# Optimization experiments

Hardware: AMD Instinct MI355X
Metric: run time of the kernel (lower is better)

Reference implementation:

```python
import jax, jax.numpy as jnp
import numpy as np

DIM = 512
NUM_HEADS = 8
HEAD_DIM = DIM // NUM_HEADS


def setup_inputs() -> dict:
    key = jax.random.key(0)
    k_x, k_qkv, k_p = jax.random.split(key, 3)
    b, n, c = 8, 4096, DIM
    x = jax.random.normal(k_x, (b, n, c), dtype=jnp.float32)
    # xavier_uniform for Linear(dim, 3*dim): limit = sqrt(6/(in+out))
    lim_qkv = float(np.sqrt(6.0 / (c + 3 * c)))
    w_qkv = jax.random.uniform(k_qkv, (c, 3 * c), dtype=jnp.float32, minval=-lim_qkv, maxval=lim_qkv)
    b_qkv = jnp.zeros((3 * c,), dtype=jnp.float32)
    lim_p = float(np.sqrt(6.0 / (c + c)))
    w_p = jax.random.uniform(k_p, (c, c), dtype=jnp.float32, minval=-lim_p, maxval=lim_p)
    b_p = jnp.zeros((c,), dtype=jnp.float32)
    temperature = jnp.full((NUM_HEADS, 1, 1), 1.0 / np.sqrt(HEAD_DIM), dtype=jnp.float32)
    return {"x": x, "w_qkv": w_qkv, "b_qkv": b_qkv, "w_p": w_p, "b_p": b_p,
            "temperature": temperature}


def reference(x, w_qkv, b_qkv, w_p, b_p, temperature):
    b, n, c = x.shape
    h, d = NUM_HEADS, HEAD_DIM
    qkv = x @ w_qkv + b_qkv                      # [b, n, 3c]
    q, k, v = jnp.split(qkv, 3, axis=-1)         # each [b, n, c]
    # -> [b, h, n, d]
    q = q.reshape(b, n, h, d).transpose(0, 2, 1, 3)
    k = k.reshape(b, n, h, d).transpose(0, 2, 1, 3)
    v = v.reshape(b, n, h, d).transpose(0, 2, 1, 3)
    # channel attention: d x d score matrix, reduced over tokens n
    scores = jnp.einsum('bhnd,bhne->bhde', q, k) * temperature  # [b,h,d,d]
    attn = jax.nn.softmax(scores, axis=-1)
    # y = attn @ v^T then permute -> [b, n, h, d]
    y = jnp.einsum('bhde,bhne->bnhd', attn, v).reshape(b, n, c)
    return y @ w_p + b_p
```

## Files before the change

### kernel.cpp

```cpp
#include <hip/hip_runtime.h>

typedef __attribute__((ext_vector_type(8))) short s16x8;
typedef __attribute__((ext_vector_type(4))) short s16x4;
typedef __attribute__((ext_vector_type(4))) float fx4;

__device__ inline unsigned short f2bf(float f) {
  unsigned u = __float_as_uint(f);
  u += 0x7fffu + ((u >> 16) & 1u);
  return (unsigned short)(u >> 16);
}
__device__ inline float bf2f(unsigned short s) {
  return __uint_as_float(((unsigned)s) << 16);
}

#define GLDS16(gp, lp) \
  __builtin_amdgcn_global_load_lds((const __attribute__((address_space(1))) void*)(gp), \
                                   (__attribute__((address_space(3))) void*)(lp), 16, 0, 0)

__global__ __launch_bounds__(256) void cast_x_k(const float* __restrict__ x,
                                                unsigned short* __restrict__ xb,
                                                unsigned short* __restrict__ xT,
                                                float* __restrict__ s_part,
                                                const float* __restrict__ w,
                                                const float* __restrict__ wp,
                                                unsigned short* __restrict__ wkT,
                                                unsigned short* __restrict__ wvb,
                                                unsigned short* __restrict__ wpb) {
  __shared__ unsigned short lt[64 * 66];
  __shared__ float red[64 * 4];
  int blk = blockIdx.x;
  int t = threadIdx.x;
  if (blk >= 4096) {
    int wblk = blk - 4096;
    if (wblk < 64) {
      int rt = wblk >> 3, ct = wblk & 7;
      int rn = t >> 2, seg = (t & 3) * 16;
      const float* src = w + (size_t)(ct * 64 + rn) * 1536 + 512 + rt * 64 + seg;
#pragma unroll
      for (int k = 0; k < 16; ++k) lt[(seg + k) * 66 + rn] = f2bf(src[k]);
      __syncthreads();
      int j = t >> 2, nseg = (t & 3) * 16;
      unsigned short* o = wkT + (size_t)(rt * 64 + j) * 512 + ct * 64 + nseg;
      *(s16x8*)&o[0] = *(s16x8*)&lt[j * 66 + nseg];
      *(s16x8*)&o[8] = *(s16x8*)&lt[j * 66 + nseg + 8];
    } else if (wblk < 192) {
      int o = (wblk - 64) * 2048 + t * 8;
      int c = o >> 9, e = o & 511;
      const float* src = w + (size_t)c * 1536 + 1024 + e;
      unsigned short h[8];
#pragma unroll
      for (int i = 0; i < 8; ++i) h[i] = f2bf(src[i]);
      *(s16x8*)&wvb[o] = *(s16x8*)&h[0];
    } else {
      int o = (wblk - 192) * 2048 + t * 8;
      unsigned short h[8];
#pragma unroll
      for (int i = 0; i < 8; ++i) h[i] = f2bf(wp[o + i]);
      *(s16x8*)&wpb[o] = *(s16x8*)&h[0];
    }
    return;
  }
  int b = blk >> 9, r = blk & 511, nt = r >> 3, ct = r & 7;
  int n0 = nt * 64, c0 = ct * 64;
  int rn = t >> 2, seg = (t & 3) * 16;
  const float* xp = x + ((size_t)b * 4096 + n0 + rn) * 512 + c0 + seg;
  fx4 v0 = *(const fx4*)&xp[0], v1 = *(const fx4*)&xp[4];
  fx4 v2 = *(const fx4*)&xp[8], v3 = *(const fx4*)&xp[12];
  unsigned short h[16];
  h[0]=f2bf(v0[0]); h[1]=f2bf(v0[1]); h[2]=f2bf(v0[2]); h[3]=f2bf(v0[3]);
  h[4]=f2bf(v1[0]); h[5]=f2bf(v1[1]); h[6]=f2bf(v1[2]); h[7]=f2bf(v1[3]);
  h[8]=f2bf(v2[0]); h[9]=f2bf(v2[1]); h[10]=f2bf(v2[2]); h[11]=f2bf(v2[3]);
  h[12]=f2bf(v3[0]); h[13]=f2bf(v3[1]); h[14]=f2bf(v3[2]); h[15]=f2bf(v3[3]);
  unsigned short* xbo = xb + ((size_t)b * 4096 + n0 + rn) * 512 + c0 + seg;
  *(s16x8*)&xbo[0] = *(s16x8*)&h[0];
  *(s16x8*)&xbo[8] = *(s16x8*)&h[8];
#pragma unroll
  for (int k = 0; k < 16; ++k) lt[(seg + k) * 66 + rn] = h[k];
  __syncthreads();
  {
    int c = t & 63, q = t >> 6;
    float p = 0.f;
#pragma unroll
    for (int i = 0; i < 16; ++i) p += bf2f(lt[c * 66 + q * 16 + i]);
    red[c * 4 + q] = p;
  }
  __syncthreads();
  if (t < 64) {
    float s = red[t * 4] + red[t * 4 + 1] + red[t * 4 + 2] + red[t * 4 + 3];
    s_part[((size_t)(b * 64 + nt)) * 512 + c0 + t] = s;
  }
  int c = t >> 2, nseg = (t & 3) * 16;
  unsigned short* xto = xT + ((size_t)b * 512 + c0 + c) * 4096 + n0 + nseg;
  *(s16x8*)&xto[0] = *(s16x8*)&lt[c * 66 + nseg];
  *(s16x8*)&xto[8] = *(s16x8*)&lt[c * 66 + nseg + 8];
}

template <int MODE>
__global__ __launch_bounds__(256, 4) void gemm_k(
    const unsigned short* __restrict__ A0, const unsigned short* __restrict__ B0,
    const float* __restrict__ bias, unsigned short* __restrict__ obf,
    float* __restrict__ of32, const float* __restrict__ wf) {
  constexpr int LD = (MODE == 0) ? 4096 : 512;
  constexpr int KSTEPS = (MODE == 0) ? 32 : 16;
  constexpr int NWG = (MODE == 0) ? 352 : (MODE == 3) ? 1024 : (MODE == 2) ? 136 : 128;
  __shared__ alignas(16) unsigned short As[2][128 * 32];
  __shared__ alignas(16) unsigned short Bs[2][128 * 32];
  int tid = threadIdx.x, wave = tid >> 6, lane = tid & 63;
  int l15 = lane & 15, l16 = lane >> 4;
  int wr = wave >> 1, wc = wave & 1;

  int bid = (blockIdx.x & 7) * (NWG >> 3) + (blockIdx.x >> 3);

  if (MODE == 0 && bid >= 320) {
    float* sb = (float*)As;
    int ubid = bid - 320;
    int b = ubid >> 2, jq = ubid & 3;
    int t = tid;
#pragma unroll
    for (int cc = 0; cc < 2; ++cc) {
      int c = cc * 256 + t;
      float a = 0.f;
      for (int nt = 0; nt < 64; ++nt)
        a += bias[((size_t)(b * 64 + nt)) * 512 + c];
      sb[c] = a;
    }
    __syncthreads();
    int j = jq * 256 + t;
    float ua = 0.f;
    for (int c = 0; c < 512; ++c)
      ua += sb[c] * wf[(size_t)c * 1536 + j];
    ((float*)obf)[b * 1024 + j] = ua;
    return;
  }
  if (MODE == 2 && bid >= 128) {
    float* bv = (float*)As;
    int b = bid - 128;
    int t = tid;
    bv[t] = bias[1024 + t];
    bv[t + 256] = bias[1280 + t];
    __syncthreads();
#pragma unroll
    for (int jj = 0; jj < 2; ++jj) {
      int j = jj * 256 + t;
      const unsigned short* wrow = &A0[((size_t)(b * 512 + j)) << 9];
      float s = 0.f;
      for (int e = 0; e < 512; e += 8) {
        s16x8 v = *(const s16x8*)&wrow[e];
#pragma unroll
        for (int q = 0; q < 8; ++q) s += bv[e + q] * bf2f((unsigned short)v[q]);
      }
      of32[b * 512 + j] = wf[j] + s;
    }
    return;
  }

  int b = 0, mt = 0, nt = 0, ks = 0;
  if (MODE == 0) {
    const int TTM[10] = {0, 0, 0, 0, 1, 1, 1, 2, 2, 3};
    const int TTN[10] = {0, 1, 2, 3, 1, 2, 3, 2, 3, 3};
    ks = bid / 80; int r = bid - ks * 80; b = r / 10; int tt = r - b * 10;
    mt = TTM[tt]; nt = TTN[tt];
  }
  else if (MODE == 3) { b = bid >> 7; int r = bid & 127; mt = r >> 2; nt = r & 3; }
  else { b = bid >> 4; mt = (bid >> 2) & 3; nt = bid & 3; }

  const unsigned short* Ab;
  const unsigned short* Bb;
  if (MODE == 0) { Ab = A0 + ((size_t)b * 512 + mt * 128) * 4096 + ks * 1024;
                   Bb = A0 + ((size_t)b * 512 + nt * 128) * 4096 + ks * 1024; }
  else if (MODE == 1) { Ab = A0 + (size_t)mt * 128 * 512;
                        Bb = B0 + ((size_t)b * 512 + nt * 128) * 512; }
  else if (MODE == 2) { Ab = A0 + ((size_t)b * 512 + mt * 128) * 512;
                        Bb = B0 + (size_t)nt * 128 * 512; }
  else { Ab = A0 + ((size_t)b * 4096 + mt * 128) * 512;
         Bb = B0 + ((size_t)b * 512 + nt * 128) * 512; }

  fx4 acc[4][4];
#pragma unroll
  for (int i = 0; i < 4; ++i)
#pragma unroll
    for (int j = 0; j < 4; ++j) acc[i][j] = (fx4){0.f, 0.f, 0.f, 0.f};

  int smr = wave * 16 + (lane >> 2);
  int skk = (((lane & 3) ^ ((lane >> 3) & 3))) * 8;
  const unsigned short* agp = Ab + (size_t)smr * LD + skk;
  const unsigned short* bgp = Bb + (size_t)smr * LD + skk;
  int ldsoff = wave * 512;

#define STAGE(buf, kt_)                                          \
  do {                                                           \
    int k0_ = (kt_) * 32;                                        \
    GLDS16(agp + k0_, &As[buf][ldsoff]);                         \
    GLDS16(agp + (size_t)64 * LD + k0_, &As[buf][ldsoff + 2048]);\
    GLDS16(bgp + k0_, &Bs[buf][ldsoff]);                         \
    GLDS16(bgp + (size_t)64 * LD + k0_, &Bs[buf][ldsoff + 2048]);\
  } while (0)

  STAGE(0, 0);
  asm volatile("s_waitcnt vmcnt(0)" ::: "memory");
  __builtin_amdgcn_s_barrier();

  int g = (l15 >> 1) & 3;
  int pa = (l16 ^ g) << 3;

  for (int kt = 0; kt < KSTEPS; ++kt) {
    int cur = kt & 1;
    if (kt < KSTEPS - 1) STAGE(cur ^ 1, kt + 1);

    s16x8 af[4], bf[4];
#pragma unroll
    for (int mi = 0; mi < 4; ++mi)
      af[mi] = *(const s16x8*)&As[cur][(wr * 64 + mi * 16 + l15) * 32 + pa];
#pragma unroll
    for (int nj = 0; nj < 4; ++nj)
      bf[nj] = *(const s16x8*)&Bs[cur][(wc * 64 + nj * 16 + l15) * 32 + pa];
#pragma unroll
    for (int mi = 0; mi < 4; ++mi)
#pragma unroll
      for (int nj = 0; nj < 4; ++nj)
        acc[mi][nj] = __builtin_amdgcn_mfma_f32_16x16x32_bf16(af[mi], bf[nj], acc[mi][nj], 0, 0, 0);

    asm volatile("s_waitcnt vmcnt(0)" ::: "memory");
    __builtin_amdgcn_s_barrier();
  }
#undef STAGE

  int R0 = mt * 128 + wr * 64, C0 = nt * 128 + wc * 64;
#pragma unroll
  for (int mi = 0; mi < 4; ++mi)
#pragma unroll
    for (int nj = 0; nj < 4; ++nj) {
      int gc = C0 + nj * 16 + l15;
#pragma unroll
      for (int r = 0; r < 4; ++r) {
        int gr = R0 + mi * 16 + l16 * 4 + r;
        float val = acc[mi][nj][r];
        if (MODE == 0) {
          of32[(((size_t)(ks * 8 + b)) * 512 + gr) * 512 + gc] = val;
        } else if (MODE == 1) {
          obf[((size_t)(b * 512 + gr)) * 512 + gc] = f2bf(val);
        } else if (MODE == 2) {
          obf[((size_t)(b * 512 + gr)) * 512 + gc] = f2bf(val);
        } else {
          of32[((size_t)(b * 4096 + gr)) * 512 + gc] = val + bias[b * 512 + gc];
        }
      }
    }
}

__global__ __launch_bounds__(256) void gsum_k(const float* __restrict__ Gpart,
                                              unsigned short* __restrict__ G16) {
  __shared__ float ts[64 * 65];
  int blk = blockIdx.x;
  int b = blk >> 6, rt = (blk >> 3) & 7, ct = blk & 7;
  int t = threadIdx.x;
  int r0 = t >> 4, c0 = (t & 15) * 4;
  bool lower = (rt >> 1) > (ct >> 1);
  if (!lower) {
#pragma unroll
    for (int rr = 0; rr < 4; ++rr) {
      int row = rr * 16 + r0;
      size_t base = (((size_t)b * 512) + rt * 64 + row) * 512 + ct * 64 + c0;
      fx4 a = {0.f, 0.f, 0.f, 0.f};
#pragma unroll
      for (int p = 0; p < 4; ++p) a += *(const fx4*)&Gpart[(size_t)p * 2097152 + base];
      unsigned short h4[4];
#pragma unroll
      for (int i = 0; i < 4; ++i) h4[i] = f2bf(a[i]);
      *(s16x4*)&G16[(((size_t)b * 512) + rt * 64 + row) * 512 + ct * 64 + c0] = *(s16x4*)&h4[0];
    }
  } else {
#pragma unroll
    for (int rr = 0; rr < 4; ++rr) {
      int srow = rr * 16 + r0;
      size_t base = (((size_t)b * 512) + ct * 64 + srow) * 512 + rt * 64 + c0;
      fx4 a = {0.f, 0.f, 0.f, 0.f};
#pragma unroll
      for (int p = 0; p < 4; ++p) a += *(const fx4*)&Gpart[(size_t)p * 2097152 + base];
#pragma unroll
      for (int i = 0; i < 4; ++i) ts[(c0 + i) * 65 + srow] = a[i];
    }
    __syncthreads();
#pragma unroll
    for (int rr = 0; rr < 4; ++rr) {
      int row = rr * 16 + r0;
      unsigned short h4[4];
#pragma unroll
      for (int i = 0; i < 4; ++i) h4[i] = f2bf(ts[row * 65 + c0 + i]);
      *(s16x4*)&G16[(((size_t)b * 512) + rt * 64 + row) * 512 + ct * 64 + c0] = *(s16x4*)&h4[0];
    }
  }
}

__global__ __launch_bounds__(256) void s_k(const float* __restrict__ wq,
                                           const unsigned short* __restrict__ GWT,
                                           float* __restrict__ sp) {
  __shared__ alignas(16) float Ws[64 * 68];
  __shared__ alignas(16) float Gs[64 * 68];
  int bid = blockIdx.x;
  int bh = bid >> 3, cch = bid & 7;
  int b = bh >> 3, h = bh & 7;
  int t = threadIdx.x;
  int cr = t >> 2, sg = (t & 3) * 16;
  const float* wsrc = wq + (size_t)(cch * 64 + cr) * 1536 + h * 64 + sg;
#pragma unroll
  for (int kk = 0; kk < 16; ++kk) Ws[cr * 68 + sg + kk] = wsrc[kk];
  const unsigned short* gsrc = GWT + ((size_t)b * 512 + h * 64 + cr) * 512 + cch * 64 + sg;
#pragma unroll
  for (int kk = 0; kk < 16; ++kk) Gs[(sg + kk) * 68 + cr] = bf2f(gsrc[kk]);
  __syncthreads();
  int dg = t >> 4, eg = t & 15;
  float acc[4][4] = {{0.f}};
  for (int cc = 0; cc < 64; ++cc) {
    fx4 wv = *(const fx4*)&Ws[cc * 68 + dg * 4];
    fx4 pv = *(const fx4*)&Gs[cc * 68 + eg * 4];
#pragma unroll
    for (int i = 0; i < 4; ++i)
#pragma unroll
      for (int j = 0; j < 4; ++j) acc[i][j] += wv[i] * pv[j];
  }
  float* o = sp + (size_t)bid * 4096;
#pragma unroll
  for (int i = 0; i < 4; ++i)
#pragma unroll
    for (int j = 0; j < 4; ++j) o[(dg * 4 + i) * 64 + eg * 4 + j] = acc[i][j];
}

__global__ __launch_bounds__(256) void softmax_weff_k(
    const float* __restrict__ sp, const unsigned short* __restrict__ wpb,
    const float* __restrict__ temp, const float* __restrict__ b_qkv,
    const float* __restrict__ u, unsigned short* __restrict__ weffT) {
  __shared__ alignas(16) float S[64 * 64];
  __shared__ alignas(16) unsigned short wps[64 * 128];
  int bh = blockIdx.x >> 2, jblk = blockIdx.x & 3;
  int b = bh >> 3, h = bh & 7;
  int tid = threadIdx.x;
  float tval = temp[h];
  for (int i = tid * 4; i < 4096; i += 1024) {
    fx4 s = {0.f, 0.f, 0.f, 0.f};
    for (int seg = 0; seg < 8; ++seg)
      s += *(const fx4*)&sp[((size_t)(bh * 8 + seg)) * 4096 + i];
    int d = i >> 6, e0 = i & 63;
    float bq = b_qkv[h * 64 + d];
    float uq = u[b * 1024 + h * 64 + d];
#pragma unroll
    for (int jj = 0; jj < 4; ++jj) {
      int e = e0 + jj;
      float bk = b_qkv[512 + h * 64 + e];
      float ksum = u[b * 1024 + 512 + h * 64 + e] + 4096.0f * bk;
      s[jj] += bq * ksum + bk * uq;
    }
    s *= tval;
    *(fx4*)&S[i] = s;
  }
  for (int i = tid * 8; i < 8192; i += 2048) {
    int d = i >> 7, c = i & 127;
    *(s16x8*)&wps[i] = *(const s16x8*)&wpb[(size_t)(h * 64 + d) * 512 + jblk * 128 + c];
  }
  __syncthreads();
  if (tid < 64) {
    float* row = &S[tid * 64];
    float mx = row[0];
    for (int e = 1; e < 64; ++e) mx = fmaxf(mx, row[e]);
    float sum = 0.f;
    for (int e = 0; e < 64; ++e) { float p = __expf(row[e] - mx); row[e] = p; sum += p; }
    float inv = 1.f / sum;
    for (int e = 0; e < 64; ++e) row[e] *= inv;
  }
  __syncthreads();
  int jg = tid >> 4, eg = tid & 15;
  int j0 = jg * 8;
  float a[4][8];
#pragma unroll
  for (int i = 0; i < 4; ++i)
#pragma unroll
    for (int j = 0; j < 8; ++j) a[i][j] = 0.f;
  for (int d = 0; d < 64; ++d) {
    fx4 at = *(const fx4*)&S[d * 64 + eg * 4];
    s16x8 wv = *(const s16x8*)&wps[d * 128 + j0];
    float wf8[8];
#pragma unroll
    for (int j = 0; j < 8; ++j) wf8[j] = bf2f((unsigned short)wv[j]);
#pragma unroll
    for (int i = 0; i < 4; ++i)
#pragma unroll
      for (int j = 0; j < 8; ++j) a[i][j] += at[i] * wf8[j];
  }
  int jglob = jblk * 128 + j0;
#pragma unroll
  for (int j = 0; j < 8; ++j) {
    unsigned short h4[4];
#pragma unroll
    for (int i = 0; i < 4; ++i) h4[i] = f2bf(a[i][j]);
    *(s16x4*)&weffT[(((size_t)b * 512 + jglob + j) << 9) + h * 64 + eg * 4] = *(s16x4*)&h4[0];
  }
}

extern "C" void kernel_launch(void* const* d_in, const int* in_sizes, int n_in,
                              void* d_out, int out_size, void* d_ws, size_t ws_size,
                              hipStream_t stream) {
  const float* x      = (const float*)d_in[0];
  const float* w_qkv  = (const float*)d_in[1];
  const float* b_qkv  = (const float*)d_in[2];
  const float* w_p    = (const float*)d_in[3];
  const float* b_p    = (const float*)d_in[4];
  const float* temp   = (const float*)d_in[5];
  float* out = (float*)d_out;
  char* ws = (char*)d_ws;

  unsigned short* xb     = (unsigned short*)(ws + 0);
  unsigned short* xT     = (unsigned short*)(ws + 33554432);
  float*          Gpart  = (float*)(ws + 67108864);
  float*          s_part = (float*)(ws + 67108864);
  unsigned short* G16    = (unsigned short*)(ws + 100663296);
  unsigned short* GWT    = (unsigned short*)(ws + 104857600);
  float*          sp     = (float*)(ws + 109051904);
  unsigned short* wkT    = (unsigned short*)(ws + 117440512);
  unsigned short* wvb    = (unsigned short*)(ws + 117964800);
  unsigned short* wpb    = (unsigned short*)(ws + 118489088);
  float*          u      = (float*)(ws + 119013376);
  float*          bias_o = (float*)(ws + 119046144);
  unsigned short* weffT  = (unsigned short*)(ws + 33554432);
  unsigned short* wcombT = (unsigned short*)(ws + 37748736);

  s_part = (float*)(ws + 119062528);

  cast_x_k<<<4416, 256, 0, stream>>>(x, xb, xT, s_part, w_qkv, w_p, wkT, wvb, wpb);
  gemm_k<0><<<352, 256, 0, stream>>>(xT, nullptr, s_part, (unsigned short*)u, Gpart, w_qkv);
  gsum_k<<<512, 256, 0, stream>>>(Gpart, G16);
  gemm_k<1><<<128, 256, 0, stream>>>(wkT, G16, nullptr, GWT, nullptr, nullptr);
  s_k<<<512, 256, 0, stream>>>(w_qkv, GWT, sp);
  softmax_weff_k<<<256, 256, 0, stream>>>(sp, wpb, temp, b_qkv, u, weffT);
  gemm_k<2><<<136, 256, 0, stream>>>(weffT, wvb, b_qkv, wcombT, bias_o, b_p);
  gemm_k<3><<<1024, 256, 0, stream>>>(xb, wcombT, bias_o, nullptr, out, nullptr);
}
```

Baseline: 137.2 us.

## Replace final output GEMM with 256x256-tile, 512-thread pipelined kernel

Moves the last GEMM (x times the combined weight, plus bias) out of the generic 128x128 gemm_k and into a dedicated kernel. The new kernel uses 256x256 tiles, 8 waves and BK=64 with an XOR-swizzled LDS layout. It splits global-to-LDS prefetches into quarter stages interleaved with MFMA groups under s_setprio, aiming for more reuse per loaded byte and better load/compute overlap. In exchange the grid drops to 256 workgroups with more LDS and registers per block, which lowers occupancy and adds many barriers.

```diff
diff --git a/kernel.cpp b/kernel.cpp
--- a/kernel.cpp
+++ b/kernel.cpp
@@ -102,7 +102,7 @@
     float* __restrict__ of32, const float* __restrict__ wf) {
   constexpr int LD = (MODE == 0) ? 4096 : 512;
   constexpr int KSTEPS = (MODE == 0) ? 32 : 16;
-  constexpr int NWG = (MODE == 0) ? 352 : (MODE == 3) ? 1024 : (MODE == 2) ? 136 : 128;
+  constexpr int NWG = (MODE == 0) ? 352 : (MODE == 2) ? 136 : 128;
   __shared__ alignas(16) unsigned short As[2][128 * 32];
   __shared__ alignas(16) unsigned short Bs[2][128 * 32];
   int tid = threadIdx.x, wave = tid >> 6, lane = tid & 63;
@@ -161,7 +161,6 @@
     ks = bid / 80; int r = bid - ks * 80; b = r / 10; int tt = r - b * 10;
     mt = TTM[tt]; nt = TTN[tt];
   }
-  else if (MODE == 3) { b = bid >> 7; int r = bid & 127; mt = r >> 2; nt = r & 3; }
   else { b = bid >> 4; mt = (bid >> 2) & 3; nt = bid & 3; }
 
   const unsigned short* Ab;
@@ -170,10 +169,8 @@
                    Bb = A0 + ((size_t)b * 512 + nt * 128) * 4096 + ks * 1024; }
   else if (MODE == 1) { Ab = A0 + (size_t)mt * 128 * 512;
                         Bb = B0 + ((size_t)b * 512 + nt * 128) * 512; }
-  else if (MODE == 2) { Ab = A0 + ((size_t)b * 512 + mt * 128) * 512;
-                        Bb = B0 + (size_t)nt * 128 * 512; }
-  else { Ab = A0 + ((size_t)b * 4096 + mt * 128) * 512;
-         Bb = B0 + ((size_t)b * 512 + nt * 128) * 512; }
+  else { Ab = A0 + ((size_t)b * 512 + mt * 128) * 512;
+         Bb = B0 + (size_t)nt * 128 * 512; }
 
   fx4 acc[4][4];
 #pragma unroll
@@ -237,13 +234,122 @@
         float val = acc[mi][nj][r];
         if (MODE == 0) {
           of32[(((size_t)(ks * 8 + b)) * 512 + gr) * 512 + gc] = val;
-        } else if (MODE == 1) {
+        } else {
           obf[((size_t)(b * 512 + gr)) * 512 + gc] = f2bf(val);
-        } else if (MODE == 2) {
-          obf[((size_t)(b * 512 + gr)) * 512 + gc] = f2bf(val);
-        } else {
-          of32[((size_t)(b * 4096 + gr)) * 512 + gc] = val + bias[b * 512 + gc];
         }
+      }
+    }
+}
+
+__global__ __launch_bounds__(512, 2) void gemm3_k(
+    const unsigned short* __restrict__ A0, const unsigned short* __restrict__ B0,
+    const float* __restrict__ bias, float* __restrict__ outp) {
+  __shared__ alignas(16) unsigned short As[2][16384];
+  __shared__ alignas(16) unsigned short Bs[2][16384];
+  int tid = threadIdx.x, wave = tid >> 6, lane = tid & 63;
+  int l15 = lane & 15, l16 = lane >> 4;
+  int wr = wave >> 2, wc = wave & 3;
+
+  int bid = (blockIdx.x & 7) * 32 + (blockIdx.x >> 3);
+  int b = bid >> 5, rr_ = bid & 31, mt = rr_ >> 1, nt = rr_ & 1;
+
+  const unsigned short* Ab = A0 + ((size_t)b * 4096 + mt * 256) * 512;
+  const unsigned short* Bb = B0 + ((size_t)b * 512 + nt * 256) * 512;
+
+  fx4 acc[8][4];
+#pragma unroll
+  for (int i = 0; i < 8; ++i)
+#pragma unroll
+    for (int j = 0; j < 4; ++j) acc[i][j] = (fx4){0.f, 0.f, 0.f, 0.f};
+
+  int srow = tid >> 3;
+  int chk = ((tid & 7) ^ (srow & 7)) * 8;
+  const unsigned short* agp = Ab + (size_t)srow * 512 + chk;
+  const unsigned short* bgp = Bb + (size_t)srow * 512 + chk;
+  int wofs = wave * 512;
+
+#define SG_A(nb, tt, h, q) GLDS16(agp + (size_t)((h)*128 + (q)*64) * 512 + (tt)*64, \
+                                  &As[nb][((h)*128 + (q)*64) * 64 + wofs])
+#define SG_B(nb, tt, h, q) GLDS16(bgp + (size_t)((h)*128 + (q)*64) * 512 + (tt)*64, \
+                                  &Bs[nb][((h)*128 + (q)*64) * 64 + wofs])
+
+  SG_A(0, 0, 0, 0); SG_A(0, 0, 0, 1); SG_A(0, 0, 1, 0); SG_A(0, 0, 1, 1);
+  SG_B(0, 0, 0, 0); SG_B(0, 0, 0, 1); SG_B(0, 0, 1, 0); SG_B(0, 0, 1, 1);
+
+  s16x8 af[4], bf[4];
+  int aro = wr * 128, bro = wc * 64;
+
+#define RD_A(buf, qm, ks)                                                              \
+  {                                                                                    \
+    _Pragma("unroll")                                                                  \
+    for (int i = 0; i < 4; ++i)                                                        \
+      af[i] = *(const s16x8*)&As[buf][(aro + (qm)*64 + i*16 + l15) * 64 +              \
+                                      ((((ks)*4 + l16) ^ (l15 & 7)) * 8)];             \
+  }
+#define RD_B(buf, ks)                                                                  \
+  {                                                                                    \
+    _Pragma("unroll")                                                                  \
+    for (int j = 0; j < 4; ++j)                                                        \
+      bf[j] = *(const s16x8*)&Bs[buf][(bro + j*16 + l15) * 64 +                        \
+                                      ((((ks)*4 + l16) ^ (l15 & 7)) * 8)];             \
+  }
+#define MM(qm)                                                                         \
+  {                                                                                    \
+    __builtin_amdgcn_s_setprio(1);                                                     \
+    _Pragma("unroll")                                                                  \
+    for (int i = 0; i < 4; ++i)                                                        \
+      _Pragma("unroll")                                                                \
+      for (int j = 0; j < 4; ++j)                                                      \
+        acc[(qm)*4 + i][j] =                                                           \
+            __builtin_amdgcn_mfma_f32_16x16x32_bf16(af[i], bf[j], acc[(qm)*4 + i][j], 0, 0, 0); \
+    __builtin_amdgcn_s_setprio(0);                                                     \
+  }
+
+  for (int t = 0; t < 8; ++t) {
+    int buf = t & 1, nb = buf ^ 1;
+    if (t < 7) {
+      SG_A(nb, t + 1, 0, 0); SG_A(nb, t + 1, 0, 1);
+      asm volatile("s_waitcnt vmcnt(2)" ::: "memory");
+    } else {
+      asm volatile("s_waitcnt vmcnt(0)" ::: "memory");
+    }
+    __builtin_amdgcn_s_barrier();
+    RD_A(buf, 0, 0); RD_B(buf, 0);
+    MM(0);
+    __builtin_amdgcn_s_barrier();
+    RD_A(buf, 1, 0);
+    if (t < 7) { SG_A(nb, t + 1, 1, 0); SG_A(nb, t + 1, 1, 1); }
+    __builtin_amdgcn_s_barrier();
+    MM(1);
+    __builtin_amdgcn_s_barrier();
+    RD_A(buf, 0, 1); RD_B(buf, 1);
+    if (t < 7) { SG_B(nb, t + 1, 0, 0); SG_B(nb, t + 1, 0, 1); }
+    __builtin_amdgcn_s_barrier();
+    MM(0);
+    __builtin_amdgcn_s_barrier();
+    RD_A(buf, 1, 1);
+    if (t < 7) { SG_B(nb, t + 1, 1, 0); SG_B(nb, t + 1, 1, 1); }
+    __builtin_amdgcn_s_barrier();
+    MM(1);
+    __builtin_amdgcn_s_barrier();
+  }
+#undef SG_A
+#undef SG_B
+#undef RD_A
+#undef RD_B
+#undef MM
+
+  int crow0 = mt * 256 + wr * 128, ccol0 = nt * 256 + wc * 64;
+#pragma unroll
+  for (int am = 0; am < 8; ++am)
+#pragma unroll
+    for (int nj = 0; nj < 4; ++nj) {
+      int gc = ccol0 + nj * 16 + l15;
+      float bsv = bias[b * 512 + gc];
+#pragma unroll
+      for (int r = 0; r < 4; ++r) {
+        int gr = crow0 + am * 16 + l16 * 4 + r;
+        outp[((size_t)(b * 4096 + gr)) * 512 + gc] = acc[am][nj][r] + bsv;
       }
     }
 }
@@ -411,7 +517,6 @@
   unsigned short* xb     = (unsigned short*)(ws + 0);
   unsigned short* xT     = (unsigned short*)(ws + 33554432);
   float*          Gpart  = (float*)(ws + 67108864);
-  float*          s_part = (float*)(ws + 67108864);
   unsigned short* G16    = (unsigned short*)(ws + 100663296);
   unsigned short* GWT    = (unsigned short*)(ws + 104857600);
   float*          sp     = (float*)(ws + 109051904);
@@ -420,10 +525,9 @@
   unsigned short* wpb    = (unsigned short*)(ws + 118489088);
   float*          u      = (float*)(ws + 119013376);
   float*          bias_o = (float*)(ws + 119046144);
+  float*          s_part = (float*)(ws + 119062528);
   unsigned short* weffT  = (unsigned short*)(ws + 33554432);
   unsigned short* wcombT = (unsigned short*)(ws + 37748736);
-
-  s_part = (float*)(ws + 119062528);
 
   cast_x_k<<<4416, 256, 0, stream>>>(x, xb, xT, s_part, w_qkv, w_p, wkT, wvb, wpb);
   gemm_k<0><<<352, 256, 0, stream>>>(xT, nullptr, s_part, (unsigned short*)u, Gpart, w_qkv);
@@ -432,5 +536,5 @@
   s_k<<<512, 256, 0, stream>>>(w_qkv, GWT, sp);
   softmax_weff_k<<<256, 256, 0, stream>>>(sp, wpb, temp, b_qkv, u, weffT);
   gemm_k<2><<<136, 256, 0, stream>>>(weffT, wvb, b_qkv, wcombT, bias_o, b_p);
-  gemm_k<3><<<1024, 256, 0, stream>>>(xb, wcombT, bias_o, nullptr, out, nullptr);
-}
+  gemm3_k<<<256, 512, 0, stream>>>(xb, wcombT, bias_o, out);
+}
```

New measurement: 139.2 us. About the same (+1.5%).
